# Kernel optimization log

Hardware: AMD Instinct MI355X
Metric: run time of the kernel (lower is better)

## Reference

```python
import jax, jax.numpy as jnp
from jax import lax
import numpy as np

B, S, H, DIN, BIN, NH, NL = 32, 256, 256, 16, 2, 8, 3
DH = H // NH


def setup_inputs() -> dict:
    key = jax.random.key(0)
    it = iter(jax.random.split(key, 40))
    def nrm(shape, s=0.05):
        return jax.random.normal(next(it), shape, jnp.float32) * s
    return {
        "parts": jax.random.normal(next(it), (B, S, DIN), jnp.float32),
        "bin_info": jax.random.normal(next(it), (B, BIN), jnp.float32),
        "target": jax.random.randint(next(it), (B, S), 0, S, dtype=jnp.int32),
        "pe_W1": nrm((H // 2, DIN)), "pe_b1": jnp.zeros((H // 2,), jnp.float32),
        "pe_W2": nrm((H // 2, H // 2)), "pe_b2": jnp.zeros((H // 2,), jnp.float32),
        "be_W1": nrm((H // 4, BIN)), "be_b1": jnp.zeros((H // 4,), jnp.float32),
        "be_W2": nrm((H // 4, H // 4)), "be_b2": jnp.zeros((H // 4,), jnp.float32),
        "pos_emb": nrm((S, H // 4)),
        "tr_Wqkv": nrm((NL, 3 * H, H)), "tr_bqkv": jnp.zeros((NL, 3 * H), jnp.float32),
        "tr_Wo": nrm((NL, H, H)), "tr_bo": jnp.zeros((NL, H), jnp.float32),
        "tr_ln1_g": jnp.ones((NL, H), jnp.float32), "tr_ln1_b": jnp.zeros((NL, H), jnp.float32),
        "tr_ff_W1": nrm((NL, 2 * H, H)), "tr_ff_b1": jnp.zeros((NL, 2 * H), jnp.float32),
        "tr_ff_W2": nrm((NL, H, 2 * H)), "tr_ff_b2": jnp.zeros((NL, H), jnp.float32),
        "tr_ln2_g": jnp.ones((NL, H), jnp.float32), "tr_ln2_b": jnp.zeros((NL, H), jnp.float32),
        "lstm_Wih": nrm((4 * H, H)), "lstm_Whh": nrm((4 * H, H)),
        "lstm_bih": jnp.zeros((4 * H,), jnp.float32), "lstm_bhh": jnp.zeros((4 * H,), jnp.float32),
        "ptr_W": nrm((H, H)), "ptr_b": jnp.zeros((H,), jnp.float32),
        "ptr_v": nrm((H,)),
    }


def _ln(x, g, b):
    m = x.mean(-1, keepdims=True)
    v = ((x - m) ** 2).mean(-1, keepdims=True)
    return (x - m) / jnp.sqrt(v + 1e-5) * g + b


def _forward(parts, bin_info, target, pe_W1, pe_b1, pe_W2, pe_b2,
             be_W1, be_b1, be_W2, be_b2, pos_emb,
             tr_Wqkv, tr_bqkv, tr_Wo, tr_bo, tr_ln1_g, tr_ln1_b,
             tr_ff_W1, tr_ff_b1, tr_ff_W2, tr_ff_b2, tr_ln2_g, tr_ln2_b,
             lstm_Wih, lstm_Whh, lstm_bih, lstm_bhh, ptr_W, ptr_b, ptr_v):
    # --- encode_inputs (dropout inactive in eval) ---
    p = jax.nn.relu(parts @ pe_W1.T + pe_b1) @ pe_W2.T + pe_b2            # [B,S,H/2]
    bb = jax.nn.relu(bin_info @ be_W1.T + be_b1) @ be_W2.T + be_b2        # [B,H/4]
    bb = jnp.broadcast_to(bb[:, None, :], (B, S, H // 4))
    pe = jnp.broadcast_to(pos_emb[None], (B, S, H // 4))
    x = jnp.concatenate([p, bb, pe], axis=-1)                             # [B,S,H]
    scale = 1.0 / np.sqrt(DH)
    for l in range(NL):  # post-norm TransformerEncoderLayer, relu FFN
        qkv = x @ tr_Wqkv[l].T + tr_bqkv[l]
        q, k, v = jnp.split(qkv, 3, axis=-1)
        q = q.reshape(B, S, NH, DH).transpose(0, 2, 1, 3)
        k = k.reshape(B, S, NH, DH).transpose(0, 2, 1, 3)
        v = v.reshape(B, S, NH, DH).transpose(0, 2, 1, 3)
        a = jax.nn.softmax(jnp.einsum('bhqd,bhkd->bhqk', q, k) * scale, axis=-1)
        o = jnp.einsum('bhqk,bhkd->bhqd', a, v).transpose(0, 2, 1, 3).reshape(B, S, H)
        x = _ln(x + o @ tr_Wo[l].T + tr_bo[l], tr_ln1_g[l], tr_ln1_b[l])
        ff = jax.nn.relu(x @ tr_ff_W1[l].T + tr_ff_b1[l]) @ tr_ff_W2[l].T + tr_ff_b2[l]
        x = _ln(x + ff, tr_ln2_g[l], tr_ln2_b[l])
    enc = x
    # Note: the original's inner MultiheadAttention calls never feed the
    # returned step_logits (part_logit is overwritten), so the faithful output is
    # logits[b,t,i] = v . tanh(ptr(h_t) + ptr(enc_i)), vectorized over i here.
    e_proj = enc @ ptr_W.T + ptr_b                                        # [B,S,H]
    bidx = jnp.arange(B)

    def step(carry, tgt_t):
        h, c, xin = carry
        g = xin @ lstm_Wih.T + lstm_bih + h @ lstm_Whh.T + lstm_bhh
        i, f, gg, o = jnp.split(g, 4, axis=-1)
        c = jax.nn.sigmoid(f) * c + jax.nn.sigmoid(i) * jnp.tanh(gg)
        h = jax.nn.sigmoid(o) * jnp.tanh(c)
        hp = h @ ptr_W.T + ptr_b                                          # [B,H]
        logits = jnp.tanh(hp[:, None, :] + e_proj) @ ptr_v                # [B,S]
        nxt = enc[bidx, tgt_t]                                            # teacher forcing
        return (h, c, nxt), logits

    z = jnp.zeros((B, H), jnp.float32)
    _, logits = lax.scan(step, (z, z, z), target.T)                       # [S,B,S]
    return logits.transpose(1, 0, 2)                                      # [B,S,S]


def reference(parts, bin_info, target, pe_W1, pe_b1, pe_W2, pe_b2,
              be_W1, be_b1, be_W2, be_b2, pos_emb,
              tr_Wqkv, tr_bqkv, tr_Wo, tr_bo, tr_ln1_g, tr_ln1_b,
              tr_ff_W1, tr_ff_b1, tr_ff_W2, tr_ff_b2, tr_ln2_g, tr_ln2_b,
              lstm_Wih, lstm_Whh, lstm_bih, lstm_bhh, ptr_W, ptr_b, ptr_v):
    return _forward(parts, bin_info, target, pe_W1, pe_b1, pe_W2, pe_b2,
                    be_W1, be_b1, be_W2, be_b2, pos_emb,
                    tr_Wqkv, tr_bqkv, tr_Wo, tr_bo, tr_ln1_g, tr_ln1_b,
                    tr_ff_W1, tr_ff_b1, tr_ff_W2, tr_ff_b2, tr_ln2_g, tr_ln2_b,
                    lstm_Wih, lstm_Whh, lstm_bih, lstm_bhh, ptr_W, ptr_b, ptr_v)
```

## Files before the change

kernel.cpp:

```cpp
#include <hip/hip_runtime.h>
#include <cstddef>

#define DEV __device__ __forceinline__

DEV float fexp2(float x) { return __builtin_amdgcn_exp2f(x); }
DEV float frcp(float x)  { return __builtin_amdgcn_rcpf(x); }
DEV float fsigm(float x) { return frcp(1.0f + fexp2(-1.44269504f * x)); }
DEV float ftanh_(float x){ return 1.0f - 2.0f * frcp(1.0f + fexp2(2.88539008f * x)); }

typedef _Float16 h2t __attribute__((ext_vector_type(2)));
typedef _Float16 v8h __attribute__((ext_vector_type(8)));
typedef float v4f __attribute__((ext_vector_type(4)));
union U32H2 { unsigned int u; h2t h; };
DEV h2t u2h(unsigned int u) { U32H2 x; x.u = u; return x.h; }

template <int BM, int BN, bool RELU, bool OUTF16>
__global__ __launch_bounds__(256) void hgemm_kernel(
    const _Float16* __restrict__ A, const _Float16* __restrict__ W,
    const float* __restrict__ bias1, const float* __restrict__ bias2,
    void* __restrict__ Cout, int M, int N, int K)
{
    constexpr int MT = BM / 32;
    constexpr int NT = BN / 32;
    constexpr int RA = BM / 64;
    constexpr int RB = BN / 64;
    __shared__ _Float16 As[BM * 32];
    __shared__ _Float16 Bs[BN * 32];

    const int tid = threadIdx.x;
    const int lane = tid & 63;
    const int lm = lane & 15, lq = lane >> 4;
    const int wrow = ((tid >> 6) & 1) * (BM / 2);
    const int wcol = (tid >> 7) * (BN / 2);
    const int m0 = blockIdx.x * BM, n0 = blockIdx.y * BN;
    const _Float16* Ab = A + (size_t)m0 * K;
    const _Float16* Wb = W + (size_t)n0 * K;

    v4f acc[MT][NT];
#pragma unroll
    for (int i = 0; i < MT; ++i)
#pragma unroll
        for (int j = 0; j < NT; ++j) acc[i][j] = (v4f){0.f, 0.f, 0.f, 0.f};

    const int rowS = tid >> 2, qS = tid & 3;

    uint4 ra[RA], rb[RB];
#pragma unroll
    for (int r = 0; r < RA; ++r)
        ra[r] = *(const uint4*)(Ab + (size_t)(rowS + 64 * r) * K + qS * 8);
#pragma unroll
    for (int r = 0; r < RB; ++r)
        rb[r] = *(const uint4*)(Wb + (size_t)(rowS + 64 * r) * K + qS * 8);

    for (int k0 = 0; k0 < K; k0 += 32) {
        __syncthreads();
#pragma unroll
        for (int r = 0; r < RA; ++r)
            *(uint4*)(As + (size_t)(tid + 256 * r) * 8) = ra[r];
#pragma unroll
        for (int r = 0; r < RB; ++r)
            *(uint4*)(Bs + (size_t)(tid + 256 * r) * 8) = rb[r];
        __syncthreads();
        int kn = k0 + 32;
        if (kn < K) {
#pragma unroll
            for (int r = 0; r < RA; ++r)
                ra[r] = *(const uint4*)(Ab + (size_t)(rowS + 64 * r) * K + kn + qS * 8);
#pragma unroll
            for (int r = 0; r < RB; ++r)
                rb[r] = *(const uint4*)(Wb + (size_t)(rowS + 64 * r) * K + kn + qS * 8);
        }
        v8h af[MT], bf[NT];
#pragma unroll
        for (int i = 0; i < MT; ++i)
            af[i] = *(const v8h*)(As + (size_t)(wrow + i * 16 + lm) * 32 + lq * 8);
#pragma unroll
        for (int j = 0; j < NT; ++j)
            bf[j] = *(const v8h*)(Bs + (size_t)(wcol + j * 16 + lm) * 32 + lq * 8);
#pragma unroll
        for (int i = 0; i < MT; ++i)
#pragma unroll
            for (int j = 0; j < NT; ++j)
                acc[i][j] = __builtin_amdgcn_mfma_f32_16x16x32_f16(
                    af[i], bf[j], acc[i][j], 0, 0, 0);
    }

#pragma unroll
    for (int j = 0; j < NT; ++j) {
        int col = n0 + wcol + j * 16 + lm;
        float bv = bias1[col];
        if (bias2) bv += bias2[col];
#pragma unroll
        for (int i = 0; i < MT; ++i) {
            int rbase = m0 + wrow + i * 16 + lq * 4;
#pragma unroll
            for (int rg = 0; rg < 4; ++rg) {
                float vv = acc[i][j][rg] + bv;
                if (RELU) vv = fmaxf(vv, 0.f);
                if (OUTF16)
                    ((_Float16*)Cout)[(size_t)(rbase + rg) * N + col] = (_Float16)vv;
                else
                    ((float*)Cout)[(size_t)(rbase + rg) * N + col] = vv;
            }
        }
    }
}

__global__ __launch_bounds__(256) void cvt_all_kernel(
    const float* __restrict__ s0, const float* __restrict__ s1,
    const float* __restrict__ s2, const float* __restrict__ s3,
    const float* __restrict__ s4, const float* __restrict__ s5,
    _Float16* __restrict__ dst)
{
    int i = blockIdx.x * 256 + threadIdx.x;
    if (i >= 1900544) return;
    float val;
    if (i < 589824)       val = s0[i];
    else if (i < 786432)  val = s1[i - 589824];
    else if (i < 1179648) val = s2[i - 786432];
    else if (i < 1572864) val = s3[i - 1179648];
    else if (i < 1835008) {
        int idx = i - 1572864;
        int rp = idx >> 8, k = idx & 255;
        int j = rp >> 2, g = rp & 3;
        val = s4[(g * 256 + j) * 256 + k];
    }
    else                  val = s5[i - 1835008];
    dst[i] = (_Float16)val;
}

__global__ __launch_bounds__(64) void bin_enc_kernel(
    const float* __restrict__ bin_info, const float* __restrict__ W1,
    const float* __restrict__ b1, const float* __restrict__ W2,
    const float* __restrict__ b2, float* __restrict__ BBo)
{
    int b = blockIdx.x, d = threadIdx.x;
    __shared__ float h1[64];
    float x0 = bin_info[b * 2], x1 = bin_info[b * 2 + 1];
    h1[d] = fmaxf(W1[d * 2] * x0 + W1[d * 2 + 1] * x1 + b1[d], 0.f);
    __syncthreads();
    float acc = b2[d];
#pragma unroll 4
    for (int e = 0; e < 64; ++e) acc += W2[d * 64 + e] * h1[e];
    BBo[b * 64 + d] = acc;
}

__global__ __launch_bounds__(128) void part_enc_kernel(
    const float* __restrict__ parts, const float* __restrict__ W1,
    const float* __restrict__ b1, const float* __restrict__ W2,
    const float* __restrict__ b2, const float* __restrict__ BBi,
    const float* __restrict__ pos_emb, float* __restrict__ X,
    _Float16* __restrict__ X16)
{
    __shared__ float W2s[128][129];
    __shared__ float h1[128];
    __shared__ float pin[16];
    int tid = threadIdx.x;
    int b = blockIdx.x >> 3, s0 = (blockIdx.x & 7) * 32;
    for (int l = 0; l < 128; ++l) W2s[l][tid] = W2[l * 128 + tid];
    float w1r[16];
#pragma unroll
    for (int k = 0; k < 16; ++k) w1r[k] = W1[tid * 16 + k];
    float bias1v = b1[tid], bias2v = b2[tid];
    for (int si = 0; si < 32; ++si) {
        int s = s0 + si;
        size_t row = (size_t)b * 256 + s;
        if (tid < 16) pin[tid] = parts[row * 16 + tid];
        __syncthreads();
        float h = bias1v;
#pragma unroll
        for (int k = 0; k < 16; ++k) h += w1r[k] * pin[k];
        h1[tid] = fmaxf(h, 0.f);
        __syncthreads();
        float acc = bias2v;
#pragma unroll 4
        for (int e = 0; e < 128; ++e) acc += W2s[tid][e] * h1[e];
        X[row * 256 + tid] = acc;
        X16[row * 256 + tid] = (_Float16)acc;
        if (tid < 64) {
            float bbv = BBi[b * 64 + tid];
            float pev = pos_emb[s * 64 + tid];
            X[row * 256 + 128 + tid] = bbv;
            X[row * 256 + 192 + tid] = pev;
            X16[row * 256 + 128 + tid] = (_Float16)bbv;
            X16[row * 256 + 192 + tid] = (_Float16)pev;
        }
        __syncthreads();
    }
}

__global__ __launch_bounds__(256) void attn_mfma_kernel(
    const _Float16* __restrict__ QKV, _Float16* __restrict__ O16)
{
    int bh = blockIdx.x;
    int b = bh >> 3, h = bh & 7;
    const int tid = threadIdx.x;
    const int w = tid >> 6;
    const int lane = tid & 63;
    const int lm = lane & 15, lq = lane >> 4;
    const float c_se = 0.17677669529663687f * 1.44269504f;

    __shared__ _Float16 Ks[4][256][8];
    __shared__ _Float16 Vt[32][264];
    __shared__ _Float16 Ps[4][16][264];

    const _Float16* qkvb = QKV + (size_t)(b * 256) * 768 + h * 32;
    {
        int s = tid;
        const _Float16* kr = qkvb + (size_t)s * 768 + 256;
#pragma unroll
        for (int c = 0; c < 4; ++c)
            *(uint4*)&Ks[c][s][0] = *(const uint4*)(kr + c * 8);
        const _Float16* vr = qkvb + (size_t)s * 768 + 512;
        _Float16 vtmp[32];
        *(uint4*)&vtmp[0]  = *(const uint4*)(vr);
        *(uint4*)&vtmp[8]  = *(const uint4*)(vr + 8);
        *(uint4*)&vtmp[16] = *(const uint4*)(vr + 16);
        *(uint4*)&vtmp[24] = *(const uint4*)(vr + 24);
#pragma unroll
        for (int d = 0; d < 32; ++d) Vt[d][s] = vtmp[d];
    }
    __syncthreads();

#pragma unroll 1
    for (int st = 0; st < 4; ++st) {
        int rt = w * 4 + st;
        v8h qf = *(const v8h*)(QKV + (size_t)(b * 256 + rt * 16 + lm) * 768
                               + h * 32 + lq * 8);
        v4f acc[16];
#pragma unroll
        for (int ct = 0; ct < 16; ++ct) {
            v8h kf = *(const v8h*)&Ks[lq][ct * 16 + lm][0];
            acc[ct] = __builtin_amdgcn_mfma_f32_16x16x32_f16(
                qf, kf, (v4f){0.f, 0.f, 0.f, 0.f}, 0, 0, 0);
        }
        float sminv[4];
#pragma unroll
        for (int r = 0; r < 4; ++r) {
            float m = acc[0][r];
#pragma unroll
            for (int ct = 1; ct < 16; ++ct) m = fmaxf(m, acc[ct][r]);
#pragma unroll
            for (int msk = 1; msk < 16; msk <<= 1)
                m = fmaxf(m, __shfl_xor(m, msk));
            float ssum = 0.f;
#pragma unroll
            for (int ct = 0; ct < 16; ++ct) {
                float e = fexp2((acc[ct][r] - m) * c_se);
                acc[ct][r] = e;
                ssum += e;
            }
#pragma unroll
            for (int msk = 1; msk < 16; msk <<= 1)
                ssum += __shfl_xor(ssum, msk);
            sminv[r] = frcp(ssum);
        }
#pragma unroll
        for (int ct = 0; ct < 16; ++ct)
#pragma unroll
            for (int r = 0; r < 4; ++r)
                Ps[w][lq * 4 + r][ct * 16 + lm] =
                    (_Float16)(acc[ct][r] * sminv[r]);
#pragma unroll
        for (int dt = 0; dt < 2; ++dt) {
            v4f o = (v4f){0.f, 0.f, 0.f, 0.f};
#pragma unroll
            for (int jc = 0; jc < 8; ++jc) {
                v8h pf = *(const v8h*)&Ps[w][lm][jc * 32 + lq * 8];
                v8h vf = *(const v8h*)&Vt[dt * 16 + lm][jc * 32 + lq * 8];
                o = __builtin_amdgcn_mfma_f32_16x16x32_f16(pf, vf, o, 0, 0, 0);
            }
#pragma unroll
            for (int r = 0; r < 4; ++r)
                O16[(size_t)(b * 256 + rt * 16 + lq * 4 + r) * 256
                    + h * 32 + dt * 16 + lm] = (_Float16)o[r];
        }
    }
}

__global__ __launch_bounds__(256) void add_ln_kernel(
    float* __restrict__ X, const float* __restrict__ R,
    const float* __restrict__ g, const float* __restrict__ beta,
    _Float16* __restrict__ X16)
{
    int row = blockIdx.x * 4 + (threadIdx.x >> 6);
    int lane = threadIdx.x & 63;
    size_t base = (size_t)row * 256 + lane * 4;
    float4 xv = *(const float4*)&X[base];
    float4 rv = *(const float4*)&R[base];
    float y0 = xv.x + rv.x, y1 = xv.y + rv.y;
    float y2 = xv.z + rv.z, y3 = xv.w + rv.w;
    float s = y0 + y1 + y2 + y3;
    float s2 = y0 * y0 + y1 * y1 + y2 * y2 + y3 * y3;
#pragma unroll
    for (int m = 1; m < 64; m <<= 1) {
        s += __shfl_xor(s, m);
        s2 += __shfl_xor(s2, m);
    }
    float mean = s * (1.f / 256.f);
    float var = s2 * (1.f / 256.f) - mean * mean;
    float inv = rsqrtf(var + 1e-5f);
    float4 gv = *(const float4*)&g[lane * 4];
    float4 bv = *(const float4*)&beta[lane * 4];
    float o0 = (y0 - mean) * inv * gv.x + bv.x;
    float o1 = (y1 - mean) * inv * gv.y + bv.y;
    float o2 = (y2 - mean) * inv * gv.z + bv.z;
    float o3 = (y3 - mean) * inv * gv.w + bv.w;
    *(float4*)&X[base] = make_float4(o0, o1, o2, o3);
    U32H2 a, c;
    a.h = h2t{(_Float16)o0, (_Float16)o1};
    c.h = h2t{(_Float16)o2, (_Float16)o3};
    uint2 u; u.x = a.u; u.y = c.u;
    *(uint2*)(X16 + base) = u;
}

__global__ __launch_bounds__(256) void gather_kernel(
    const float* __restrict__ X, const int* __restrict__ target,
    _Float16* __restrict__ Xg16)
{
    int row = blockIdx.x;
    int b = row >> 8, t = row & 255;
    int d = threadIdx.x;
    float val = 0.f;
    if (t > 0) {
        int src = target[b * 256 + t - 1];
        val = X[((size_t)b * 256 + src) * 256 + d];
    }
    Xg16[(size_t)row * 256 + d] = (_Float16)val;
}

__global__ __launch_bounds__(256) void wcvt2_kernel(
    const float* __restrict__ Whh, unsigned int* __restrict__ WB,
    const float* __restrict__ bih, const float* __restrict__ bhh,
    float* __restrict__ PB)
{
    int idx = blockIdx.x * 256 + threadIdx.x;
    if (idx < 1024) {
        int j = idx >> 2, g = idx & 3;
        PB[idx] = bih[g * 256 + j] + bhh[g * 256 + j];
    }
    int l = idx & 3;
    int gt = idx >> 2;
    int tid = gt & 511;
    int q = gt >> 9;
    int i, c;
    if (q < 8)       { i = q >> 1; c = q & 1; }
    else if (q < 52) { int qq = q - 8; i = qq / 11; c = 2 + qq % 11; }
    else             { int qq = q - 52; c = 13 + (qq >> 2); i = qq & 3; }
    int r = ((tid & 255) << 2) + i;
    int k = ((tid >> 8) << 7) + (c << 3) + (l << 1);
    _Float16 lo = (_Float16)Whh[r * 256 + k];
    _Float16 hi = (_Float16)Whh[r * 256 + k + 1];
    U32H2 x; x.h = h2t{lo, hi};
    WB[idx] = x.u;
}

__global__ __launch_bounds__(512) void lstm_kernel(
    const _Float16* __restrict__ g_in, const uint4* __restrict__ WB4,
    _Float16* __restrict__ HALL16)
{
    const int b = blockIdx.x;
    const int tid = threadIdx.x;
    const int kh = tid >> 8, j4 = tid & 255;

    __shared__ uint4 WL4[4096];
    __shared__ float gpart[2][1024];
    __shared__ uint4 h2v[32];
    unsigned int* h2_s = (unsigned int*)h2v;

#pragma unroll
    for (int g = 0; g < 8; ++g) WL4[g * 512 + tid] = WB4[g * 512 + tid];
    uint4 wr[44];
#pragma unroll
    for (int q = 0; q < 44; ++q) wr[q] = WB4[(8 + q) * 512 + tid];
    if (tid < 128) h2_s[tid] = 0u;

    const _Float16* ginb = g_in + (size_t)b * 256 * 1024;
    uint2 gi = make_uint2(0u, 0u);
    if (tid < 256) gi = *(const uint2*)(ginb + tid * 4);
    float c_state = 0.f;
    const uint4* SW4 = WB4 + 52 * 512;
    __syncthreads();

    for (int t = 0; t < 256; ++t) {
        uint4 sw[12];
#pragma unroll
        for (int q = 0; q < 4; ++q) sw[q] = SW4[q * 512 + tid];

        float acc[4] = {0.f, 0.f, 0.f, 0.f};
#pragma unroll
        for (int c = 0; c < 16; ++c) {
            if (c == 2) {
#pragma unroll
                for (int q = 4; q < 8; ++q) sw[q] = SW4[q * 512 + tid];
            }
            if (c == 6) {
#pragma unroll
                for (int q = 8; q < 12; ++q) sw[q] = SW4[q * 512 + tid];
            }
            uint4 h4 = h2v[(kh << 4) + c];
            h2t hx = u2h(h4.x), hy = u2h(h4.y), hz = u2h(h4.z), hw = u2h(h4.w);
#pragma unroll
            for (int i = 0; i < 4; ++i) {
                uint4 w = (c < 2)  ? WL4[((i << 1) + c) * 512 + tid]
                        : (c < 13) ? wr[i * 11 + (c - 2)]
                                   : sw[((c - 13) << 2) + i];
                acc[i] = __builtin_amdgcn_fdot2(u2h(w.x), hx, acc[i], false);
                acc[i] = __builtin_amdgcn_fdot2(u2h(w.y), hy, acc[i], false);
                acc[i] = __builtin_amdgcn_fdot2(u2h(w.z), hz, acc[i], false);
                acc[i] = __builtin_amdgcn_fdot2(u2h(w.w), hw, acc[i], false);
            }
        }
        *(float4*)&gpart[kh][j4 << 2] = make_float4(acc[0], acc[1], acc[2], acc[3]);
        __syncthreads();

        if (tid < 256) {
            int j = tid;
            h2t p0 = u2h(gi.x), p1 = u2h(gi.y);
            float ig = (float)p0.x + gpart[0][j]       + gpart[1][j];
            float fg = (float)p0.y + gpart[0][j + 256] + gpart[1][j + 256];
            float gg = (float)p1.x + gpart[0][j + 512] + gpart[1][j + 512];
            float og = (float)p1.y + gpart[0][j + 768] + gpart[1][j + 768];
            c_state = fsigm(fg) * c_state + fsigm(ig) * ftanh_(gg);
            float h = fsigm(og) * ftanh_(c_state);
            HALL16[((size_t)(b * 256 + t)) * 256 + j] = (_Float16)h;
            U32H2 hxp; hxp.h = h2t{(_Float16)h, (_Float16)0.f};
            unsigned int hu = hxp.u & 0xffffu;
            unsigned int other = (unsigned int)__shfl_xor((int)hu, 1);
            if ((j & 1) == 0) h2_s[j >> 1] = hu | (other << 16);
            int tn = (t < 255) ? (t + 1) : 255;
            gi = *(const uint2*)(ginb + (size_t)tn * 1024 + j * 4);
        }
        __syncthreads();
    }
}

__global__ __launch_bounds__(256) void pointer_kernel(
    const float* __restrict__ HP, const float* __restrict__ EP,
    const float* __restrict__ v, float* __restrict__ out)
{
    int b = blockIdx.z, tt = blockIdx.y, it = blockIdx.x;
    __shared__ float hp_s[16][260];
    __shared__ float ep_s[16][260];
    __shared__ float v_s[256];
    __shared__ float red[4];
    int tid = threadIdx.x;
    const float cs = 2.88539008f;
    const float* hpb = HP + ((size_t)b * 256 + tt * 16) * 256;
    const float* epb = EP + ((size_t)b * 256 + it * 16) * 256;
#pragma unroll
    for (int l = 0; l < 4; ++l) {
        int idx = tid + l * 256;
        int r = idx >> 6, c4 = idx & 63;
        float4 hv = *(const float4*)(hpb + r * 256 + c4 * 4);
        hv.x *= cs; hv.y *= cs; hv.z *= cs; hv.w *= cs;
        *(float4*)&hp_s[r][c4 * 4] = hv;
        float4 ev = *(const float4*)(epb + r * 256 + c4 * 4);
        ev.x *= cs; ev.y *= cs; ev.z *= cs; ev.w *= cs;
        *(float4*)&ep_s[r][c4 * 4] = ev;
    }
    float vv = v[tid];
    v_s[tid] = vv;
    float vp = vv;
#pragma unroll
    for (int m = 1; m < 64; m <<= 1) vp += __shfl_xor(vp, m);
    if ((tid & 63) == 0) red[tid >> 6] = vp;
    __syncthreads();
    float vsum = red[0] + red[1] + red[2] + red[3];
    int tl = tid >> 4, il = tid & 15;
    float acc = 0.f;
#pragma unroll 4
    for (int d = 0; d < 256; ++d) {
        float sval = hp_s[tl][d] + ep_s[il][d];
        float r = frcp(1.0f + fexp2(sval));
        acc = fmaf(v_s[d], r, acc);
    }
    out[((size_t)b * 256 + tt * 16 + tl) * 256 + it * 16 + il] =
        vsum - 2.0f * acc;
}

extern "C" void kernel_launch(void* const* d_in, const int* in_sizes, int n_in,
                              void* d_out, int out_size, void* d_ws, size_t ws_size,
                              hipStream_t stream)
{
    const float* parts    = (const float*)d_in[0];
    const float* bin_info = (const float*)d_in[1];
    const int*   target   = (const int*)d_in[2];
    const float* pe_W1 = (const float*)d_in[3];
    const float* pe_b1 = (const float*)d_in[4];
    const float* pe_W2 = (const float*)d_in[5];
    const float* pe_b2 = (const float*)d_in[6];
    const float* be_W1 = (const float*)d_in[7];
    const float* be_b1 = (const float*)d_in[8];
    const float* be_W2 = (const float*)d_in[9];
    const float* be_b2 = (const float*)d_in[10];
    const float* pos_emb = (const float*)d_in[11];
    const float* tr_Wqkv = (const float*)d_in[12];
    const float* tr_bqkv = (const float*)d_in[13];
    const float* tr_Wo   = (const float*)d_in[14];
    const float* tr_bo   = (const float*)d_in[15];
    const float* tr_ln1_g = (const float*)d_in[16];
    const float* tr_ln1_b = (const float*)d_in[17];
    const float* tr_ff_W1 = (const float*)d_in[18];
    const float* tr_ff_b1 = (const float*)d_in[19];
    const float* tr_ff_W2 = (const float*)d_in[20];
    const float* tr_ff_b2 = (const float*)d_in[21];
    const float* tr_ln2_g = (const float*)d_in[22];
    const float* tr_ln2_b = (const float*)d_in[23];
    const float* lstm_Wih = (const float*)d_in[24];
    const float* lstm_Whh = (const float*)d_in[25];
    const float* lstm_bih = (const float*)d_in[26];
    const float* lstm_bhh = (const float*)d_in[27];
    const float* ptr_W = (const float*)d_in[28];
    const float* ptr_b = (const float*)d_in[29];
    const float* ptr_v = (const float*)d_in[30];

    float* ws = (float*)d_ws;
    float* X     = ws;
    float* S1    = X + 2097152;
    float* CF32  = S1 + 8388608;
    float* EPROJ = CF32 + 2097152;
    float* X16f  = EPROJ + 2097152;
    float* S2f   = X16f + 1048576;
    float* W16f  = S2f + 1048576;
    float* WBf   = W16f + 1048576;
    float* BBuf  = WBf + 131072;
    float* PB    = BBuf + 2048;

    _Float16* X16    = (_Float16*)X16f;
    _Float16* Xg16   = X16;
    _Float16* S2h    = (_Float16*)S2f;
    _Float16* HALL16 = S2h;
    _Float16* S1h    = (_Float16*)S1;
    _Float16* W16    = (_Float16*)W16f;
    _Float16* Wqkv16 = W16;
    _Float16* Wo16   = Wqkv16 + 589824;
    _Float16* Wff116 = Wo16 + 196608;
    _Float16* Wff216 = Wff116 + 393216;
    _Float16* Wih16  = Wff216 + 393216;
    _Float16* WpW16  = Wih16 + 262144;

    cvt_all_kernel<<<7424, 256, 0, stream>>>(tr_Wqkv, tr_Wo, tr_ff_W1, tr_ff_W2,
                                             lstm_Wih, ptr_W, W16);
    wcvt2_kernel<<<512, 256, 0, stream>>>(lstm_Whh, (unsigned int*)WBf,
                                          lstm_bih, lstm_bhh, PB);

    bin_enc_kernel<<<32, 64, 0, stream>>>(bin_info, be_W1, be_b1, be_W2, be_b2, BBuf);
    part_enc_kernel<<<256, 128, 0, stream>>>(parts, pe_W1, pe_b1, pe_W2, pe_b2,
                                             BBuf, pos_emb, X, X16);

    for (int l = 0; l < 3; ++l) {
        hgemm_kernel<64, 128, false, true><<<dim3(128, 6), 256, 0, stream>>>(
            X16, Wqkv16 + (size_t)l * 196608, tr_bqkv + l * 768, nullptr,
            S1h, 8192, 768, 256);
        attn_mfma_kernel<<<256, 256, 0, stream>>>(S1h, S2h);
        hgemm_kernel<64, 64, false, false><<<dim3(128, 4), 256, 0, stream>>>(
            S2h, Wo16 + (size_t)l * 65536, tr_bo + l * 256, nullptr,
            CF32, 8192, 256, 256);
        add_ln_kernel<<<2048, 256, 0, stream>>>(X, CF32, tr_ln1_g + l * 256,
                                                tr_ln1_b + l * 256, X16);
        hgemm_kernel<64, 128, true, true><<<dim3(128, 4), 256, 0, stream>>>(
            X16, Wff116 + (size_t)l * 131072, tr_ff_b1 + l * 512, nullptr,
            S1h, 8192, 512, 256);
        hgemm_kernel<64, 64, false, false><<<dim3(128, 4), 256, 0, stream>>>(
            S1h, Wff216 + (size_t)l * 131072, tr_ff_b2 + l * 256, nullptr,
            CF32, 8192, 256, 512);
        add_ln_kernel<<<2048, 256, 0, stream>>>(X, CF32, tr_ln2_g + l * 256,
                                                tr_ln2_b + l * 256, X16);
    }

    hgemm_kernel<64, 64, false, false><<<dim3(128, 4), 256, 0, stream>>>(
        X16, WpW16, ptr_b, nullptr, EPROJ, 8192, 256, 256);
    gather_kernel<<<8192, 256, 0, stream>>>(X, target, Xg16);
    hgemm_kernel<64, 128, false, true><<<dim3(128, 8), 256, 0, stream>>>(
        Xg16, Wih16, PB, nullptr, S1h, 8192, 1024, 256);
    lstm_kernel<<<32, 512, 0, stream>>>(S1h, (const uint4*)WBf, HALL16);
    hgemm_kernel<64, 64, false, false><<<dim3(128, 4), 256, 0, stream>>>(
        HALL16, WpW16, ptr_b, nullptr, CF32, 8192, 256, 256);
    pointer_kernel<<<dim3(16, 16, 32), 256, 0, stream>>>(CF32, EPROJ, ptr_v,
                                                         (float*)d_out);
}
```

Baseline: 966.1 us.

## Replace LDS-staged GEMM with direct-load MFMA GEMM and fuse gather into input projection

The shared-memory staged GEMM is replaced by a kernel in which each wave loads its MFMA fragments straight from global memory with the K loop fully unrolled at compile time, using 64x64 tiles for every projection. This removes the LDS round trip and the __syncthreads barriers. The teacher-forcing gather is folded into the LSTM input-projection GEMM by indexing A rows through the target array, so the separate gather kernel and its intermediate buffer go away. In exchange, the gathered rows now come from the fp16 copy of the encoder output instead of the fp32 one, operands are reused less across waves, and more redundant global and L2 loads are issued.

```diff
diff --git a/kernel.cpp b/kernel.cpp
--- a/kernel.cpp
+++ b/kernel.cpp
@@ -14,84 +14,55 @@
 union U32H2 { unsigned int u; h2t h; };
 DEV h2t u2h(unsigned int u) { U32H2 x; x.u = u; return x.h; }
 
-template <int BM, int BN, bool RELU, bool OUTF16>
-__global__ __launch_bounds__(256) void hgemm_kernel(
+template <int KT, bool RELU, bool OUTF16, bool GATHER>
+__global__ __launch_bounds__(256) void dgemm_kernel(
     const _Float16* __restrict__ A, const _Float16* __restrict__ W,
-    const float* __restrict__ bias1, const float* __restrict__ bias2,
-    void* __restrict__ Cout, int M, int N, int K)
-{
-    constexpr int MT = BM / 32;
-    constexpr int NT = BN / 32;
-    constexpr int RA = BM / 64;
-    constexpr int RB = BN / 64;
-    __shared__ _Float16 As[BM * 32];
-    __shared__ _Float16 Bs[BN * 32];
-
+    const float* __restrict__ bias1, void* __restrict__ Cout,
+    int N, const int* __restrict__ target)
+{
     const int tid = threadIdx.x;
-    const int lane = tid & 63;
+    const int w = tid >> 6, lane = tid & 63;
     const int lm = lane & 15, lq = lane >> 4;
-    const int wrow = ((tid >> 6) & 1) * (BM / 2);
-    const int wcol = (tid >> 7) * (BN / 2);
-    const int m0 = blockIdx.x * BM, n0 = blockIdx.y * BN;
-    const _Float16* Ab = A + (size_t)m0 * K;
-    const _Float16* Wb = W + (size_t)n0 * K;
-
-    v4f acc[MT][NT];
-#pragma unroll
-    for (int i = 0; i < MT; ++i)
-#pragma unroll
-        for (int j = 0; j < NT; ++j) acc[i][j] = (v4f){0.f, 0.f, 0.f, 0.f};
-
-    const int rowS = tid >> 2, qS = tid & 3;
-
-    uint4 ra[RA], rb[RB];
-#pragma unroll
-    for (int r = 0; r < RA; ++r)
-        ra[r] = *(const uint4*)(Ab + (size_t)(rowS + 64 * r) * K + qS * 8);
-#pragma unroll
-    for (int r = 0; r < RB; ++r)
-        rb[r] = *(const uint4*)(Wb + (size_t)(rowS + 64 * r) * K + qS * 8);
-
-    for (int k0 = 0; k0 < K; k0 += 32) {
-        __syncthreads();
-#pragma unroll
-        for (int r = 0; r < RA; ++r)
-            *(uint4*)(As + (size_t)(tid + 256 * r) * 8) = ra[r];
-#pragma unroll
-        for (int r = 0; r < RB; ++r)
-            *(uint4*)(Bs + (size_t)(tid + 256 * r) * 8) = rb[r];
-        __syncthreads();
-        int kn = k0 + 32;
-        if (kn < K) {
-#pragma unroll
-            for (int r = 0; r < RA; ++r)
-                ra[r] = *(const uint4*)(Ab + (size_t)(rowS + 64 * r) * K + kn + qS * 8);
-#pragma unroll
-            for (int r = 0; r < RB; ++r)
-                rb[r] = *(const uint4*)(Wb + (size_t)(rowS + 64 * r) * K + kn + qS * 8);
-        }
-        v8h af[MT], bf[NT];
-#pragma unroll
-        for (int i = 0; i < MT; ++i)
-            af[i] = *(const v8h*)(As + (size_t)(wrow + i * 16 + lm) * 32 + lq * 8);
-#pragma unroll
-        for (int j = 0; j < NT; ++j)
-            bf[j] = *(const v8h*)(Bs + (size_t)(wcol + j * 16 + lm) * 32 + lq * 8);
-#pragma unroll
-        for (int i = 0; i < MT; ++i)
-#pragma unroll
-            for (int j = 0; j < NT; ++j)
-                acc[i][j] = __builtin_amdgcn_mfma_f32_16x16x32_f16(
-                    af[i], bf[j], acc[i][j], 0, 0, 0);
-    }
-
-#pragma unroll
-    for (int j = 0; j < NT; ++j) {
+    const int wrow = (w & 1) * 32, wcol = (w >> 1) * 32;
+    const int m0 = blockIdx.x * 64, n0 = blockIdx.y * 64;
+
+    int arow[2]; bool azero[2];
+#pragma unroll
+    for (int i = 0; i < 2; ++i) {
+        int r = m0 + wrow + i * 16 + lm;
+        if (GATHER) {
+            int b = r >> 8, t = r & 255;
+            if (t == 0) { azero[i] = true; arow[i] = r; }
+            else { azero[i] = false; arow[i] = (b << 8) + target[(b << 8) + t - 1]; }
+        } else { azero[i] = false; arow[i] = r; }
+    }
+    const int brow0 = n0 + wcol + lm, brow1 = n0 + wcol + 16 + lm;
+
+    v4f acc[2][2];
+    acc[0][0] = (v4f){0.f,0.f,0.f,0.f}; acc[0][1] = (v4f){0.f,0.f,0.f,0.f};
+    acc[1][0] = (v4f){0.f,0.f,0.f,0.f}; acc[1][1] = (v4f){0.f,0.f,0.f,0.f};
+    const v8h zh = {(_Float16)0,(_Float16)0,(_Float16)0,(_Float16)0,
+                    (_Float16)0,(_Float16)0,(_Float16)0,(_Float16)0};
+
+#pragma unroll
+    for (int kq = 0; kq < KT / 32; ++kq) {
+        const int ko = kq * 32 + lq * 8;
+        v8h af0 = azero[0] ? zh : *(const v8h*)(A + (size_t)arow[0] * KT + ko);
+        v8h af1 = azero[1] ? zh : *(const v8h*)(A + (size_t)arow[1] * KT + ko);
+        v8h bf0 = *(const v8h*)(W + (size_t)brow0 * KT + ko);
+        v8h bf1 = *(const v8h*)(W + (size_t)brow1 * KT + ko);
+        acc[0][0] = __builtin_amdgcn_mfma_f32_16x16x32_f16(af0, bf0, acc[0][0], 0, 0, 0);
+        acc[0][1] = __builtin_amdgcn_mfma_f32_16x16x32_f16(af0, bf1, acc[0][1], 0, 0, 0);
+        acc[1][0] = __builtin_amdgcn_mfma_f32_16x16x32_f16(af1, bf0, acc[1][0], 0, 0, 0);
+        acc[1][1] = __builtin_amdgcn_mfma_f32_16x16x32_f16(af1, bf1, acc[1][1], 0, 0, 0);
+    }
+
+#pragma unroll
+    for (int j = 0; j < 2; ++j) {
         int col = n0 + wcol + j * 16 + lm;
         float bv = bias1[col];
-        if (bias2) bv += bias2[col];
-#pragma unroll
-        for (int i = 0; i < MT; ++i) {
+#pragma unroll
+        for (int i = 0; i < 2; ++i) {
             int rbase = m0 + wrow + i * 16 + lq * 4;
 #pragma unroll
             for (int rg = 0; rg < 4; ++rg) {
@@ -312,21 +283,6 @@
     c.h = h2t{(_Float16)o2, (_Float16)o3};
     uint2 u; u.x = a.u; u.y = c.u;
     *(uint2*)(X16 + base) = u;
-}
-
-__global__ __launch_bounds__(256) void gather_kernel(
-    const float* __restrict__ X, const int* __restrict__ target,
-    _Float16* __restrict__ Xg16)
-{
-    int row = blockIdx.x;
-    int b = row >> 8, t = row & 255;
-    int d = threadIdx.x;
-    float val = 0.f;
-    if (t > 0) {
-        int src = target[b * 256 + t - 1];
-        val = X[((size_t)b * 256 + src) * 256 + d];
-    }
-    Xg16[(size_t)row * 256 + d] = (_Float16)val;
 }
 
 __global__ __launch_bounds__(256) void wcvt2_kernel(
@@ -528,7 +484,6 @@
     float* PB    = BBuf + 2048;
 
     _Float16* X16    = (_Float16*)X16f;
-    _Float16* Xg16   = X16;
     _Float16* S2h    = (_Float16*)S2f;
     _Float16* HALL16 = S2h;
     _Float16* S1h    = (_Float16*)S1;
@@ -550,33 +505,28 @@
                                              BBuf, pos_emb, X, X16);
 
     for (int l = 0; l < 3; ++l) {
-        hgemm_kernel<64, 128, false, true><<<dim3(128, 6), 256, 0, stream>>>(
-            X16, Wqkv16 + (size_t)l * 196608, tr_bqkv + l * 768, nullptr,
-            S1h, 8192, 768, 256);
+        dgemm_kernel<256, false, true, false><<<dim3(128, 12), 256, 0, stream>>>(
+            X16, Wqkv16 + (size_t)l * 196608, tr_bqkv + l * 768, S1h, 768, nullptr);
         attn_mfma_kernel<<<256, 256, 0, stream>>>(S1h, S2h);
-        hgemm_kernel<64, 64, false, false><<<dim3(128, 4), 256, 0, stream>>>(
-            S2h, Wo16 + (size_t)l * 65536, tr_bo + l * 256, nullptr,
-            CF32, 8192, 256, 256);
+        dgemm_kernel<256, false, false, false><<<dim3(128, 4), 256, 0, stream>>>(
+            S2h, Wo16 + (size_t)l * 65536, tr_bo + l * 256, CF32, 256, nullptr);
         add_ln_kernel<<<2048, 256, 0, stream>>>(X, CF32, tr_ln1_g + l * 256,
                                                 tr_ln1_b + l * 256, X16);
-        hgemm_kernel<64, 128, true, true><<<dim3(128, 4), 256, 0, stream>>>(
-            X16, Wff116 + (size_t)l * 131072, tr_ff_b1 + l * 512, nullptr,
-            S1h, 8192, 512, 256);
-        hgemm_kernel<64, 64, false, false><<<dim3(128, 4), 256, 0, stream>>>(
-            S1h, Wff216 + (size_t)l * 131072, tr_ff_b2 + l * 256, nullptr,
-            CF32, 8192, 256, 512);
+        dgemm_kernel<256, true, true, false><<<dim3(128, 8), 256, 0, stream>>>(
+            X16, Wff116 + (size_t)l * 131072, tr_ff_b1 + l * 512, S1h, 512, nullptr);
+        dgemm_kernel<512, false, false, false><<<dim3(128, 4), 256, 0, stream>>>(
+            S1h, Wff216 + (size_t)l * 131072, tr_ff_b2 + l * 256, CF32, 256, nullptr);
         add_ln_kernel<<<2048, 256, 0, stream>>>(X, CF32, tr_ln2_g + l * 256,
                                                 tr_ln2_b + l * 256, X16);
     }
 
-    hgemm_kernel<64, 64, false, false><<<dim3(128, 4), 256, 0, stream>>>(
-        X16, WpW16, ptr_b, nullptr, EPROJ, 8192, 256, 256);
-    gather_kernel<<<8192, 256, 0, stream>>>(X, target, Xg16);
-    hgemm_kernel<64, 128, false, true><<<dim3(128, 8), 256, 0, stream>>>(
-        Xg16, Wih16, PB, nullptr, S1h, 8192, 1024, 256);
+    dgemm_kernel<256, false, false, false><<<dim3(128, 4), 256, 0, stream>>>(
+        X16, WpW16, ptr_b, EPROJ, 256, nullptr);
+    dgemm_kernel<256, false, true, true><<<dim3(128, 16), 256, 0, stream>>>(
+        X16, Wih16, PB, S1h, 1024, target);
     lstm_kernel<<<32, 512, 0, stream>>>(S1h, (const uint4*)WBf, HALL16);
-    hgemm_kernel<64, 64, false, false><<<dim3(128, 4), 256, 0, stream>>>(
-        HALL16, WpW16, ptr_b, nullptr, CF32, 8192, 256, 256);
+    dgemm_kernel<256, false, false, false><<<dim3(128, 4), 256, 0, stream>>>(
+        HALL16, WpW16, ptr_b, CF32, 256, nullptr);
     pointer_kernel<<<dim3(16, 16, 32), 256, 0, stream>>>(CF32, EPROJ, ptr_v,
                                                          (float*)d_out);
 }
```

Result: slower. 1.010 ms (+4.6%).

## Retile pointer kernel with register blocking and fuse gather into LSTM input GEMM

Applied to the files above, without the earlier changes.

The pointer-score kernel moves from 16x16 tiles to 64x64 tiles with 512 threads. Each thread computes a 4x2 block of outputs from float4 LDS reads of hp and a transposed ep tile, and the factor of 2 is folded into v, which cuts LDS traffic per exp/rcp evaluation. The teacher-forcing gather kernel is removed: the LSTM input-projection GEMM now computes gathered row indices from the target and reads X16 directly, zero-filling the t=0 rows. The new pointer tile uses roughly 130KB of LDS, so only one block fits per CU, and the kernel relies on the large shared-memory size of this hardware.

```diff
diff --git a/kernel.cpp b/kernel.cpp
--- a/kernel.cpp
+++ b/kernel.cpp
@@ -14,11 +14,11 @@
 union U32H2 { unsigned int u; h2t h; };
 DEV h2t u2h(unsigned int u) { U32H2 x; x.u = u; return x.h; }
 
-template <int BM, int BN, bool RELU, bool OUTF16>
+template <int BM, int BN, bool RELU, bool OUTF16, bool GATHER>
 __global__ __launch_bounds__(256) void hgemm_kernel(
     const _Float16* __restrict__ A, const _Float16* __restrict__ W,
-    const float* __restrict__ bias1, const float* __restrict__ bias2,
-    void* __restrict__ Cout, int M, int N, int K)
+    const float* __restrict__ bias1, void* __restrict__ Cout,
+    int M, int N, int K, const int* __restrict__ target)
 {
     constexpr int MT = BM / 32;
     constexpr int NT = BN / 32;
@@ -33,7 +33,6 @@
     const int wrow = ((tid >> 6) & 1) * (BM / 2);
     const int wcol = (tid >> 7) * (BN / 2);
     const int m0 = blockIdx.x * BM, n0 = blockIdx.y * BN;
-    const _Float16* Ab = A + (size_t)m0 * K;
     const _Float16* Wb = W + (size_t)n0 * K;
 
     v4f acc[MT][NT];
@@ -44,10 +43,23 @@
 
     const int rowS = tid >> 2, qS = tid & 3;
 
+    size_t arow[RA]; bool az[RA];
+#pragma unroll
+    for (int r = 0; r < RA; ++r) {
+        int row = m0 + rowS + 64 * r;
+        if (GATHER) {
+            int b = row >> 8, t = row & 255;
+            if (t == 0) { az[r] = true; arow[r] = 0; }
+            else { az[r] = false;
+                   arow[r] = (size_t)((b << 8) + target[(b << 8) + t - 1]); }
+        } else { az[r] = false; arow[r] = (size_t)row; }
+    }
+    const uint4 z4 = {0u, 0u, 0u, 0u};
+
     uint4 ra[RA], rb[RB];
 #pragma unroll
     for (int r = 0; r < RA; ++r)
-        ra[r] = *(const uint4*)(Ab + (size_t)(rowS + 64 * r) * K + qS * 8);
+        ra[r] = az[r] ? z4 : *(const uint4*)(A + arow[r] * K + qS * 8);
 #pragma unroll
     for (int r = 0; r < RB; ++r)
         rb[r] = *(const uint4*)(Wb + (size_t)(rowS + 64 * r) * K + qS * 8);
@@ -65,7 +77,7 @@
         if (kn < K) {
 #pragma unroll
             for (int r = 0; r < RA; ++r)
-                ra[r] = *(const uint4*)(Ab + (size_t)(rowS + 64 * r) * K + kn + qS * 8);
+                ra[r] = az[r] ? z4 : *(const uint4*)(A + arow[r] * K + kn + qS * 8);
 #pragma unroll
             for (int r = 0; r < RB; ++r)
                 rb[r] = *(const uint4*)(Wb + (size_t)(rowS + 64 * r) * K + kn + qS * 8);
@@ -89,7 +101,6 @@
     for (int j = 0; j < NT; ++j) {
         int col = n0 + wcol + j * 16 + lm;
         float bv = bias1[col];
-        if (bias2) bv += bias2[col];
 #pragma unroll
         for (int i = 0; i < MT; ++i) {
             int rbase = m0 + wrow + i * 16 + lq * 4;
@@ -312,21 +323,6 @@
     c.h = h2t{(_Float16)o2, (_Float16)o3};
     uint2 u; u.x = a.u; u.y = c.u;
     *(uint2*)(X16 + base) = u;
-}
-
-__global__ __launch_bounds__(256) void gather_kernel(
-    const float* __restrict__ X, const int* __restrict__ target,
-    _Float16* __restrict__ Xg16)
-{
-    int row = blockIdx.x;
-    int b = row >> 8, t = row & 255;
-    int d = threadIdx.x;
-    float val = 0.f;
-    if (t > 0) {
-        int src = target[b * 256 + t - 1];
-        val = X[((size_t)b * 256 + src) * 256 + d];
-    }
-    Xg16[(size_t)row * 256 + d] = (_Float16)val;
 }
 
 __global__ __launch_bounds__(256) void wcvt2_kernel(
@@ -435,48 +431,81 @@
     }
 }
 
-__global__ __launch_bounds__(256) void pointer_kernel(
+__global__ __launch_bounds__(512) void pointer_kernel(
     const float* __restrict__ HP, const float* __restrict__ EP,
     const float* __restrict__ v, float* __restrict__ out)
 {
     int b = blockIdx.z, tt = blockIdx.y, it = blockIdx.x;
-    __shared__ float hp_s[16][260];
-    __shared__ float ep_s[16][260];
-    __shared__ float v_s[256];
-    __shared__ float red[4];
-    int tid = threadIdx.x;
+    __shared__ float hp_s[64][256];
+    __shared__ float ep_t[256][66];
+    __shared__ float v2_s[256];
+    __shared__ float redv[8];
+    const int tid = threadIdx.x;
     const float cs = 2.88539008f;
-    const float* hpb = HP + ((size_t)b * 256 + tt * 16) * 256;
-    const float* epb = EP + ((size_t)b * 256 + it * 16) * 256;
-#pragma unroll
-    for (int l = 0; l < 4; ++l) {
-        int idx = tid + l * 256;
+    const float* hpb = HP + ((size_t)b * 256 + tt * 64) * 256;
+    const float* epb = EP + ((size_t)b * 256 + it * 64) * 256;
+#pragma unroll
+    for (int l = 0; l < 8; ++l) {
+        int idx = tid + l * 512;
         int r = idx >> 6, c4 = idx & 63;
         float4 hv = *(const float4*)(hpb + r * 256 + c4 * 4);
         hv.x *= cs; hv.y *= cs; hv.z *= cs; hv.w *= cs;
         *(float4*)&hp_s[r][c4 * 4] = hv;
         float4 ev = *(const float4*)(epb + r * 256 + c4 * 4);
-        ev.x *= cs; ev.y *= cs; ev.z *= cs; ev.w *= cs;
-        *(float4*)&ep_s[r][c4 * 4] = ev;
-    }
-    float vv = v[tid];
-    v_s[tid] = vv;
-    float vp = vv;
+        ep_t[c4 * 4 + 0][r] = ev.x * cs;
+        ep_t[c4 * 4 + 1][r] = ev.y * cs;
+        ep_t[c4 * 4 + 2][r] = ev.z * cs;
+        ep_t[c4 * 4 + 3][r] = ev.w * cs;
+    }
+    float vp = 0.f;
+    if (tid < 256) {
+        float vv = v[tid];
+        v2_s[tid] = 2.0f * vv;
+        vp = vv;
+    }
 #pragma unroll
     for (int m = 1; m < 64; m <<= 1) vp += __shfl_xor(vp, m);
-    if ((tid & 63) == 0) red[tid >> 6] = vp;
+    if ((tid & 63) == 0) redv[tid >> 6] = vp;
     __syncthreads();
-    float vsum = red[0] + red[1] + red[2] + red[3];
-    int tl = tid >> 4, il = tid & 15;
-    float acc = 0.f;
+    float vsum = redv[0] + redv[1] + redv[2] + redv[3]
+               + redv[4] + redv[5] + redv[6] + redv[7];
+
+    const int tl = tid >> 5, il = tid & 31;
+    const int t0 = tl * 4, i0 = il * 2;
+    float acc[4][2];
+#pragma unroll
+    for (int r = 0; r < 4; ++r) { acc[r][0] = 0.f; acc[r][1] = 0.f; }
+
 #pragma unroll 4
-    for (int d = 0; d < 256; ++d) {
-        float sval = hp_s[tl][d] + ep_s[il][d];
-        float r = frcp(1.0f + fexp2(sval));
-        acc = fmaf(v_s[d], r, acc);
-    }
-    out[((size_t)b * 256 + tt * 16 + tl) * 256 + it * 16 + il] =
-        vsum - 2.0f * acc;
+    for (int dq = 0; dq < 64; ++dq) {
+        float4 h0 = *(const float4*)&hp_s[t0 + 0][dq * 4];
+        float4 h1 = *(const float4*)&hp_s[t0 + 1][dq * 4];
+        float4 h2 = *(const float4*)&hp_s[t0 + 2][dq * 4];
+        float4 h3 = *(const float4*)&hp_s[t0 + 3][dq * 4];
+        float4 vq = *(const float4*)&v2_s[dq * 4];
+        float hr[4][4] = {{h0.x, h0.y, h0.z, h0.w}, {h1.x, h1.y, h1.z, h1.w},
+                          {h2.x, h2.y, h2.z, h2.w}, {h3.x, h3.y, h3.z, h3.w}};
+        float vj[4] = {vq.x, vq.y, vq.z, vq.w};
+#pragma unroll
+        for (int j = 0; j < 4; ++j) {
+            float2 ev = *(const float2*)&ep_t[dq * 4 + j][i0];
+#pragma unroll
+            for (int r = 0; r < 4; ++r) {
+                float s0 = hr[r][j] + ev.x;
+                float s1 = hr[r][j] + ev.y;
+                acc[r][0] = fmaf(vj[j], frcp(1.0f + fexp2(s0)), acc[r][0]);
+                acc[r][1] = fmaf(vj[j], frcp(1.0f + fexp2(s1)), acc[r][1]);
+            }
+        }
+    }
+#pragma unroll
+    for (int r = 0; r < 4; ++r) {
+        float2 o;
+        o.x = vsum - acc[r][0];
+        o.y = vsum - acc[r][1];
+        *(float2*)&out[((size_t)b * 256 + tt * 64 + t0 + r) * 256
+                       + it * 64 + i0] = o;
+    }
 }
 
 extern "C" void kernel_launch(void* const* d_in, const int* in_sizes, int n_in,
@@ -528,7 +557,6 @@
     float* PB    = BBuf + 2048;
 
     _Float16* X16    = (_Float16*)X16f;
-    _Float16* Xg16   = X16;
     _Float16* S2h    = (_Float16*)S2f;
     _Float16* HALL16 = S2h;
     _Float16* S1h    = (_Float16*)S1;
@@ -550,33 +578,32 @@
                                              BBuf, pos_emb, X, X16);
 
     for (int l = 0; l < 3; ++l) {
-        hgemm_kernel<64, 128, false, true><<<dim3(128, 6), 256, 0, stream>>>(
-            X16, Wqkv16 + (size_t)l * 196608, tr_bqkv + l * 768, nullptr,
-            S1h, 8192, 768, 256);
+        hgemm_kernel<64, 128, false, true, false><<<dim3(128, 6), 256, 0, stream>>>(
+            X16, Wqkv16 + (size_t)l * 196608, tr_bqkv + l * 768,
+            S1h, 8192, 768, 256, nullptr);
         attn_mfma_kernel<<<256, 256, 0, stream>>>(S1h, S2h);
-        hgemm_kernel<64, 64, false, false><<<dim3(128, 4), 256, 0, stream>>>(
-            S2h, Wo16 + (size_t)l * 65536, tr_bo + l * 256, nullptr,
-            CF32, 8192, 256, 256);
+        hgemm_kernel<64, 64, false, false, false><<<dim3(128, 4), 256, 0, stream>>>(
+            S2h, Wo16 + (size_t)l * 65536, tr_bo + l * 256,
+            CF32, 8192, 256, 256, nullptr);
         add_ln_kernel<<<2048, 256, 0, stream>>>(X, CF32, tr_ln1_g + l * 256,
                                                 tr_ln1_b + l * 256, X16);
-        hgemm_kernel<64, 128, true, true><<<dim3(128, 4), 256, 0, stream>>>(
-            X16, Wff116 + (size_t)l * 131072, tr_ff_b1 + l * 512, nullptr,
-            S1h, 8192, 512, 256);
-        hgemm_kernel<64, 64, false, false><<<dim3(128, 4), 256, 0, stream>>>(
-            S1h, Wff216 + (size_t)l * 131072, tr_ff_b2 + l * 256, nullptr,
-            CF32, 8192, 256, 512);
+        hgemm_kernel<64, 128, true, true, false><<<dim3(128, 4), 256, 0, stream>>>(
+            X16, Wff116 + (size_t)l * 131072, tr_ff_b1 + l * 512,
+            S1h, 8192, 512, 256, nullptr);
+        hgemm_kernel<64, 64, false, false, false><<<dim3(128, 4), 256, 0, stream>>>(
+            S1h, Wff216 + (size_t)l * 131072, tr_ff_b2 + l * 256,
+            CF32, 8192, 256, 512, nullptr);
         add_ln_kernel<<<2048, 256, 0, stream>>>(X, CF32, tr_ln2_g + l * 256,
                                                 tr_ln2_b + l * 256, X16);
     }
 
-    hgemm_kernel<64, 64, false, false><<<dim3(128, 4), 256, 0, stream>>>(
-        X16, WpW16, ptr_b, nullptr, EPROJ, 8192, 256, 256);
-    gather_kernel<<<8192, 256, 0, stream>>>(X, target, Xg16);
-    hgemm_kernel<64, 128, false, true><<<dim3(128, 8), 256, 0, stream>>>(
-        Xg16, Wih16, PB, nullptr, S1h, 8192, 1024, 256);
+    hgemm_kernel<64, 64, false, false, false><<<dim3(128, 4), 256, 0, stream>>>(
+        X16, WpW16, ptr_b, EPROJ, 8192, 256, 256, nullptr);
+    hgemm_kernel<64, 128, false, true, true><<<dim3(128, 8), 256, 0, stream>>>(
+        X16, Wih16, PB, S1h, 8192, 1024, 256, target);
     lstm_kernel<<<32, 512, 0, stream>>>(S1h, (const uint4*)WBf, HALL16);
-    hgemm_kernel<64, 64, false, false><<<dim3(128, 4), 256, 0, stream>>>(
-        HALL16, WpW16, ptr_b, nullptr, CF32, 8192, 256, 256);
-    pointer_kernel<<<dim3(16, 16, 32), 256, 0, stream>>>(CF32, EPROJ, ptr_v,
-                                                         (float*)d_out);
-}
+    hgemm_kernel<64, 64, false, false, false><<<dim3(128, 4), 256, 0, stream>>>(
+        HALL16, WpW16, ptr_b, CF32, 8192, 256, 256, nullptr);
+    pointer_kernel<<<dim3(4, 4, 32), 512, 0, stream>>>(CF32, EPROJ, ptr_v,
+                                                       (float*)d_out);
+}
```

Measured after the change: 1.062 ms. +10.0%, slower.
